# Kernel tuning notes

Measured on AMD Instinct MI355X. Metric: run time of the kernel, lower is better.

The kernel has to match this reference:

```python
import jax, jax.numpy as jnp
import numpy as np

_N_JOINTS = 24
_N_VERTS = 6890
_PARENT = np.array([-1, 0, 0, 0, 1, 2, 3, 4, 5, 6, 7, 8, 9, 9, 9, 12, 13, 14, 16, 17, 18, 19, 20, 21], dtype=np.int64)


def _batch_rodrigues(rvecs):
    # rvecs: [N,3] axis-angle -> [N,3,3] rotation matrices
    angle = jnp.clip(jnp.linalg.norm(rvecs, axis=-1, keepdims=True), 1e-8, None)
    axis = rvecs / angle
    a = angle[..., 0]
    c = jnp.cos(a)
    s = jnp.sin(a)
    t = 1.0 - c
    x, y, z = axis[:, 0], axis[:, 1], axis[:, 2]
    R = jnp.stack([
        t * x * x + c, t * x * y - s * z, t * x * z + s * y,
        t * x * y + s * z, t * y * y + c, t * y * z - s * x,
        t * x * z - s * y, t * y * z + s * x, t * z * z + c,
    ], axis=-1).reshape(-1, 3, 3)
    return R


def _make_T(R, trans):
    # R: [B,J,3,3], trans: [B,J,3] -> [B,J,4,4] homogeneous transforms
    B, J = R.shape[:2]
    top = jnp.concatenate([R, trans[..., None]], axis=-1)  # [B,J,3,4]
    bottom = jnp.broadcast_to(jnp.array([0.0, 0.0, 0.0, 1.0], dtype=R.dtype), (B, J, 1, 4))
    return jnp.concatenate([top, bottom], axis=2)


def setup_inputs() -> dict:
    key = jax.random.key(0)
    ks = jax.random.split(key, 7)
    B = 1024
    theta = jax.random.normal(ks[0], (B, 72), dtype=jnp.float32) * 0.3
    beta = jax.random.normal(ks[1], (B, 10), dtype=jnp.float32)
    shapedirs = jax.random.normal(ks[2], (_N_VERTS * 3, 10), dtype=jnp.float32) * 0.01
    posedirs = jax.random.normal(ks[3], (_N_VERTS * 3, 207), dtype=jnp.float32) * 0.01
    Jreg = jax.random.uniform(ks[4], (_N_JOINTS, _N_VERTS), dtype=jnp.float32)
    Jreg = Jreg / jnp.sum(Jreg, axis=1, keepdims=True)
    v_template = jax.random.normal(ks[5], (_N_VERTS, 3), dtype=jnp.float32)
    weights = jax.random.uniform(ks[6], (_N_VERTS, _N_JOINTS), dtype=jnp.float32)
    weights = weights / jnp.sum(weights, axis=1, keepdims=True)
    return {"theta": theta, "beta": beta, "shapedirs": shapedirs, "posedirs": posedirs,
            "J_regressor": Jreg, "v_template": v_template, "weights": weights}


def reference(theta, beta, shapedirs, posedirs, J_regressor, v_template, weights):
    B = beta.shape[0]
    V = v_template.shape[0]
    # shape blendshapes
    v_shaped = v_template[None] + (beta @ shapedirs.T).reshape(B, V, 3)
    # pose rotations
    R = _batch_rodrigues(theta.reshape(-1, 3)).reshape(B, _N_JOINTS, 3, 3)
    pose_feature = (R[:, 1:] - jnp.eye(3, dtype=R.dtype)).reshape(B, -1)  # [B,207]
    v_posed = v_shaped + (pose_feature @ posedirs.T).reshape(B, V, 3)
    # joint locations
    J = jnp.einsum('jv,bvk->bjk', J_regressor, v_posed)  # [B,24,3]
    # local bone transforms (root keeps absolute translation)
    Jp = J[:, np.maximum(_PARENT, 0)]                      # [B,24,3]
    rel = J - jnp.einsum('bjkl,bjl->bjk', R, Jp)
    is_root = (jnp.arange(_N_JOINTS) == 0)[None, :, None]
    trans = jnp.where(is_root, J, rel)
    T = _make_T(R, trans)                                  # [B,24,4,4]
    # kinematic chain accumulation (fixed 24-joint tree)
    Gs = [T[:, 0]]
    for i in range(1, _N_JOINTS):
        Gs.append(jnp.matmul(Gs[int(_PARENT[i])], T[:, i]))
    G = jnp.stack(Gs, axis=1)                              # [B,24,4,4]
    # remove rest-pose joint locations
    G_rot = G[:, :, :3, :3]
    G_tr = G[:, :, :3, 3] - jnp.einsum('bjkl,bjl->bjk', G_rot, J)
    G_corr = _make_T(G_rot, G_tr)                          # [B,24,4,4]
    # linear blend skinning
    T_skin = jnp.einsum('vj,bjkl->bvkl', weights, G_corr)  # [B,V,4,4]
    v_h = jnp.concatenate([v_posed, jnp.ones((B, V, 1), dtype=v_posed.dtype)], axis=-1)
    v_out = jnp.einsum('bvkl,bvl->bvk', T_skin, v_h)[:, :, :3]
    return v_out, J
```

## Files before the change

kernel.cpp:

```cpp
#include <hip/hip_runtime.h>
#include <hip/hip_bf16.h>

#define NJ 24
#define NV 6890
#define NVP 6912
#define NR (NV*3)
#define NPF 207
#define KB 217
#define KP 256
#define NT 162
#define NT2 108
#define NSPLIT 512
#define VPB 14
#define FTILE 32768
#define FT2   49152
#define ELDW 264

typedef short s16x8 __attribute__((ext_vector_type(8)));
typedef short s16x4 __attribute__((ext_vector_type(4)));
typedef float f32x4 __attribute__((ext_vector_type(4)));
typedef float f4u   __attribute__((ext_vector_type(4), aligned(4)));

__device__ constexpr int PAR[24] = {-1,0,0,0,1,2,3,4,5,6,7,8,9,9,9,12,13,14,16,17,18,19,20,21};

__device__ __forceinline__ short f2bf(float f) {
    __hip_bfloat16 h = __float2bfloat16(f);
    return *reinterpret_cast<short*>(&h);
}
__device__ __forceinline__ float bf2fs(unsigned short u) {
    unsigned int x = ((unsigned int)u) << 16;
    return __uint_as_float(x);
}

__device__ __forceinline__ size_t frag_addr(int row128, int k) {
    int ks = k >> 5, q = (k >> 3) & 3, e = k & 7;
    int mf = row128 >> 4, r16 = row128 & 15;
    return ((size_t)(ks*8 + mf) * 64 + q*16 + r16) * 8 + e;
}

__global__ __launch_bounds__(256) void k_rodrigues(const float* __restrict__ theta,
        const float* __restrict__ beta, float* __restrict__ Rws,
        float* __restrict__ pfA, short* __restrict__ Afrag, int B) {
    int idx = blockIdx.x * blockDim.x + threadIdx.x;
    if (idx >= B * NJ) return;
    int b = idx / NJ, j = idx % NJ;
    float x = theta[b*72 + j*3 + 0];
    float y = theta[b*72 + j*3 + 1];
    float z = theta[b*72 + j*3 + 2];
    float n = sqrtf(x*x + y*y + z*z);
    float a = fmaxf(n, 1e-8f);
    float inv = 1.0f / a;
    float ix = x*inv, iy = y*inv, iz = z*inv;
    float c = cosf(a), s = sinf(a), t = 1.0f - c;
    float r[9];
    r[0] = t*ix*ix + c;     r[1] = t*ix*iy - s*iz;  r[2] = t*ix*iz + s*iy;
    r[3] = t*ix*iy + s*iz;  r[4] = t*iy*iy + c;     r[5] = t*iy*iz - s*ix;
    r[6] = t*ix*iz - s*iy;  r[7] = t*iy*iz + s*ix;  r[8] = t*iz*iz + c;
    float* Rp = Rws + (size_t)idx * 9;
    #pragma unroll
    for (int k = 0; k < 9; ++k) Rp[k] = r[k];

    int rb = b & 127;
    short* At = Afrag + (size_t)(b >> 7) * FTILE;
    float* pa = pfA + (size_t)b * 224;
    if (j >= 1) {
        #pragma unroll
        for (int kk = 0; kk < 9; ++kk) {
            int k = (j-1)*9 + kk;
            float f = r[kk] - ((kk == 0 || kk == 4 || kk == 8) ? 1.0f : 0.0f);
            At[frag_addr(rb, k)] = f2bf(f);
            pa[k] = f;
        }
    } else {
        #pragma unroll
        for (int kk = 0; kk < 10; ++kk) {
            int k = NPF + kk;
            float f = beta[b*10 + kk];
            At[frag_addr(rb, k)] = f2bf(f);
            pa[k] = f;
        }
        for (int k = KB; k < KP; ++k)
            At[frag_addr(rb, k)] = 0;
    }
}

__global__ __launch_bounds__(256) void k_convB192(const float* __restrict__ pd,
        const float* __restrict__ sd, short* __restrict__ Bf) {
    int nt = blockIdx.y;
    int id = blockIdx.x * 256 + threadIdx.x;
    int lane_ = id & 63;
    int fi = id >> 6;
    int nf = fi % 12, ks = fi / 12;
    int q = lane_ >> 4, r16 = lane_ & 15;
    int rg = nt*192 + nf*16 + r16;
    int k0 = ks*32 + q*8;
    s16x8 v;
    if (rg < NR) {
        if (k0 + 7 < NPF) {
            const float* p = pd + (size_t)rg * NPF + k0;
            #pragma unroll
            for (int k = 0; k < 8; ++k) v[k] = f2bf(p[k]);
        } else {
            #pragma unroll
            for (int k = 0; k < 8; ++k) {
                int col = k0 + k;
                float f = 0.0f;
                if (col < NPF)     f = pd[(size_t)rg * NPF + col];
                else if (col < KB) f = sd[(size_t)rg * 10 + (col - NPF)];
                v[k] = f2bf(f);
            }
        }
    } else {
        #pragma unroll
        for (int k = 0; k < 8; ++k) v[k] = 0;
    }
    *(s16x8*)&Bf[((size_t)nt * FT2) + (size_t)id * 8] = v;
}

__global__ __launch_bounds__(256) void k_convB128(const float* __restrict__ pd,
        const float* __restrict__ sd, short* __restrict__ Bf) {
    int cid = blockIdx.x * 256 + threadIdx.x;
    int lane_ = cid & 63;
    int nf = (cid >> 6) & 7;
    int ks = (cid >> 9) & 7;
    int nt = cid >> 12;
    int q = lane_ >> 4, r16 = lane_ & 15;
    int rg = nt*128 + nf*16 + r16;
    int k0 = ks*32 + q*8;
    s16x8 v;
    if (rg < NR) {
        if (k0 + 7 < NPF) {
            const float* p = pd + (size_t)rg * NPF + k0;
            #pragma unroll
            for (int k = 0; k < 8; ++k) v[k] = f2bf(p[k]);
        } else {
            #pragma unroll
            for (int k = 0; k < 8; ++k) {
                int col = k0 + k;
                float f = 0.0f;
                if (col < NPF)     f = pd[(size_t)rg * NPF + col];
                else if (col < KB) f = sd[(size_t)rg * 10 + (col - NPF)];
                v[k] = f2bf(f);
            }
        }
    } else {
        #pragma unroll
        for (int k = 0; k < 8; ++k) v[k] = 0;
    }
    *(s16x8*)&Bf[(size_t)cid * 8] = v;
}

__global__ __launch_bounds__(256) void k_jdirs(const float* __restrict__ pd,
        const float* __restrict__ sd, const float* __restrict__ vt,
        const float* __restrict__ Jreg, float* __restrict__ part) {
    __shared__ float wjs[24][VPB];
    int bi = blockIdx.x;
    int v0 = bi * VPB;
    int nv = NV - v0; if (nv > VPB) nv = VPB; if (nv < 0) nv = 0;
    for (int i = threadIdx.x; i < 24*VPB; i += 256) {
        int j = i / VPB, vv = i - j*VPB;
        wjs[j][vv] = (vv < nv) ? Jreg[(size_t)j * NV + v0 + vv] : 0.0f;
    }
    __syncthreads();
    int k = threadIdx.x;
    float acc[72];
    #pragma unroll
    for (int i = 0; i < 72; ++i) acc[i] = 0.0f;
    for (int vv = 0; vv < VPB; ++vv) {
        int v = v0 + vv;
        if (v >= NV) break;
        #pragma unroll
        for (int c = 0; c < 3; ++c) {
            int row = v*3 + c;
            float val = 0.0f;
            if (k < NPF)      val = pd[(size_t)row * NPF + k];
            else if (k < KB)  val = sd[(size_t)row * 10 + (k - NPF)];
            else if (k == KB) val = vt[row];
            #pragma unroll
            for (int j = 0; j < 24; ++j) acc[j*3 + c] += wjs[j][vv] * val;
        }
    }
    if (k < 224) {
        float* p = part + (size_t)bi * (72*224);
        #pragma unroll
        for (int i = 0; i < 72; ++i) p[i*224 + k] = acc[i];
    }
}

__global__ __launch_bounds__(256) void k_jreduce1(const float* __restrict__ part,
        float* __restrict__ part2) {
    int i = blockIdx.x;
    int s = blockIdx.y;
    int k = threadIdx.x;
    if (k >= 224) return;
    float acc = 0.0f;
    #pragma unroll 4
    for (int bi = s*64; bi < s*64 + 64; ++bi)
        acc += part[(size_t)bi * (72*224) + i*224 + k];
    part2[((size_t)s * 72 + i) * 224 + k] = acc;
}

__global__ __launch_bounds__(256) void k_jreduce2(const float* __restrict__ part2,
        float* __restrict__ JDt) {
    int e = blockIdx.x * 256 + threadIdx.x;
    if (e >= 72*224) return;
    int i = e / 224, k = e - i*224;
    float s = 0.0f;
    #pragma unroll
    for (int ss = 0; ss < 8; ++ss)
        s += part2[((size_t)ss * 72 + i) * 224 + k];
    if (k < 218) JDt[k*72 + i] = s;
}

__global__ __launch_bounds__(128) void k_J(const float* __restrict__ pfA,
        const float* __restrict__ JDt, float* __restrict__ Jout, int B) {
    int b = blockIdx.x, t = threadIdx.x;
    if (t >= 72) return;
    const float* pa = pfA + (size_t)b * 224;
    float acc = JDt[217*72 + t];
    #pragma unroll 7
    for (int k = 0; k < KB; ++k) acc += pa[k] * JDt[k*72 + t];
    Jout[(size_t)b * 72 + t] = acc;
}

__global__ __launch_bounds__(32) void k_chain(const float* __restrict__ Rg,
        const float* __restrict__ Jg, float* __restrict__ Gc, int B) {
    __shared__ float Gs[32 * 289];
    int b = blockIdx.x * 32 + threadIdx.x;
    if (b >= B) return;
    float* G = &Gs[threadIdx.x * 289];
    float Jl[72];
    const float* Jb = Jg + (size_t)b * 72;
    #pragma unroll
    for (int i = 0; i < 72; ++i) Jl[i] = Jb[i];
    const float* Rb = Rg + (size_t)b * 216;
    G[0]=Rb[0]; G[1]=Rb[1]; G[2]=Rb[2];  G[3]=Jl[0];
    G[4]=Rb[3]; G[5]=Rb[4]; G[6]=Rb[5];  G[7]=Jl[1];
    G[8]=Rb[6]; G[9]=Rb[7]; G[10]=Rb[8]; G[11]=Jl[2];
    #pragma unroll
    for (int i = 1; i < NJ; ++i) {
        const int p = PAR[i];
        const float* Ri = Rb + i*9;
        float r00=Ri[0],r01=Ri[1],r02=Ri[2];
        float r10=Ri[3],r11=Ri[4],r12=Ri[5];
        float r20=Ri[6],r21=Ri[7],r22=Ri[8];
        float px=Jl[p*3+0], py=Jl[p*3+1], pz=Jl[p*3+2];
        float tx = Jl[i*3+0] - (r00*px + r01*py + r02*pz);
        float ty = Jl[i*3+1] - (r10*px + r11*py + r12*pz);
        float tz = Jl[i*3+2] - (r20*px + r21*py + r22*pz);
        const float* gp = &G[p*12];
        float* gi = &G[i*12];
        #pragma unroll
        for (int rr = 0; rr < 3; ++rr) {
            float a0=gp[rr*4+0], a1=gp[rr*4+1], a2=gp[rr*4+2], a3=gp[rr*4+3];
            gi[rr*4+0] = a0*r00 + a1*r10 + a2*r20;
            gi[rr*4+1] = a0*r01 + a1*r11 + a2*r21;
            gi[rr*4+2] = a0*r02 + a1*r12 + a2*r22;
            gi[rr*4+3] = a0*tx + a1*ty + a2*tz + a3;
        }
    }
    float* out = Gc + (size_t)b * 288;
    #pragma unroll
    for (int i = 0; i < NJ; ++i) {
        const float* gi = &G[i*12];
        float jx=Jl[i*3+0], jy=Jl[i*3+1], jz=Jl[i*3+2];
        #pragma unroll
        for (int rr = 0; rr < 3; ++rr) {
            out[i*12+rr*4+0] = gi[rr*4+0];
            out[i*12+rr*4+1] = gi[rr*4+1];
            out[i*12+rr*4+2] = gi[rr*4+2];
            out[i*12+rr*4+3] = gi[rr*4+3] - (gi[rr*4+0]*jx + gi[rr*4+1]*jy + gi[rr*4+2]*jz);
        }
    }
}

__global__ __launch_bounds__(256) void k_gmf(const float* __restrict__ Gc,
        short* __restrict__ Gmf, int B) {
    int idx = blockIdx.x * 256 + threadIdx.x;
    if (idx >= B * 64) return;
    int lane_ = idx & 63, b = idx >> 6;
    int q = lane_ >> 4, c = lane_ & 15;
    s16x8 v;
    if (c < 12 && q < 3) {
        #pragma unroll
        for (int e = 0; e < 8; ++e)
            v[e] = f2bf(Gc[(size_t)b * 288 + (q*8 + e)*12 + c]);
    } else {
        #pragma unroll
        for (int e = 0; e < 8; ++e) v[e] = 0;
    }
    *(s16x8*)&Gmf[(size_t)idx * 8] = v;
}

__global__ __launch_bounds__(256, 2) void k_gemm(const short* __restrict__ Af,
        const short* __restrict__ Bf, const float* __restrict__ vt,
        float* __restrict__ vout, int B) {
    __shared__ float eld[64 * 128];
    const int t = threadIdx.x;
    const int wgid = blockIdx.x;
    const int bt = wgid & 7, nt = wgid >> 3;
    const int wave = t >> 6, lane = t & 63;
    const int wn = (wave & 1) * 64;
    const int q = lane >> 4, r16 = lane & 15;
    const int mfb = (wave >> 1) * 4, nfb = (wave & 1) * 4;

    const s16x8* Ab = (const s16x8*)(Af + (size_t)bt * FTILE);
    const s16x8* Bb = (const s16x8*)(Bf + (size_t)nt * FTILE);

    f32x4 acc[4][4];
    #pragma unroll
    for (int m = 0; m < 4; ++m)
        #pragma unroll
        for (int n = 0; n < 4; ++n)
            #pragma unroll
            for (int i = 0; i < 4; ++i) acc[m][n][i] = 0.0f;

    #pragma unroll
    for (int ks = 0; ks < 8; ++ks) {
        s16x8 a[4], b[4];
        #pragma unroll
        for (int m = 0; m < 4; ++m) a[m] = Ab[(ks*8 + mfb + m)*64 + lane];
        #pragma unroll
        for (int n = 0; n < 4; ++n) b[n] = Bb[(ks*8 + nfb + n)*64 + lane];
        #pragma unroll
        for (int m = 0; m < 4; ++m)
            #pragma unroll
            for (int n = 0; n < 4; ++n)
                acc[m][n] = __builtin_amdgcn_mfma_f32_16x16x32_bf16(a[m], b[n], acc[m][n], 0, 0, 0);
    }

    #pragma unroll
    for (int half = 0; half < 2; ++half) {
        if ((wave >> 1) == half) {
            #pragma unroll
            for (int m = 0; m < 4; ++m)
                #pragma unroll
                for (int n = 0; n < 4; ++n)
                    #pragma unroll
                    for (int i = 0; i < 4; ++i) {
                        int row_l = m*16 + q*4 + i;
                        int col = wn + n*16 + r16;
                        eld[row_l * 128 + (col ^ ((row_l & 7) << 2))] = acc[m][n][i];
                    }
        }
        __syncthreads();
        {
            const int c32 = t & 31;
            const int col = c32 * 4;
            const int rsub = (t >> 5) & 1;
            #pragma unroll
            for (int it = 0; it < 8; ++it) {
                int row_l = it * 8 + wave * 2 + rsub;
                int bg = bt * 128 + half * 64 + row_l;
                int rg = nt * 128 + col;
                f32x4 v = *(const f32x4*)&eld[row_l * 128 + (col ^ ((row_l & 7) << 2))];
                if (bg < B) {
                    float* dst = vout + (size_t)bg * NR + rg;
                    if (rg + 3 < NR) {
                        float4 tv = *(const float4*)(vt + rg);
                        v[0] += tv.x; v[1] += tv.y; v[2] += tv.z; v[3] += tv.w;
                        *(f4u*)dst = v;
                    } else {
                        #pragma unroll
                        for (int e = 0; e < 4; ++e)
                            if (rg + e < NR) dst[e] = v[e] + vt[rg + e];
                    }
                }
            }
        }
        __syncthreads();
    }
}

__global__ __launch_bounds__(256, 2) void k_gemm_skin(const short* __restrict__ Af,
        const short* __restrict__ Bf, const float* __restrict__ vt,
        const short* __restrict__ Gmf, const float* __restrict__ W,
        float* __restrict__ vout, int B) {
    __shared__ short elds[128 * ELDW];
    const int t = threadIdx.x;
    const int wgid = blockIdx.x;
    const int bt = wgid & 7, nt = wgid >> 3;
    const int wave = t >> 6, lane = t & 63;
    const int wn = (wave & 1) * 96;
    const int q = lane >> 4, r16 = lane & 15;
    const int mfb = (wave >> 1) * 4, nfb = (wave & 1) * 6;
    const int rowbase = (wave >> 1) * 64;

    const s16x8* Ab = (const s16x8*)(Af + (size_t)bt * FTILE);
    const s16x8* Bb = (const s16x8*)(Bf + (size_t)nt * FT2);

    f32x4 acc[4][6];
    #pragma unroll
    for (int m = 0; m < 4; ++m)
        #pragma unroll
        for (int n = 0; n < 6; ++n)
            #pragma unroll
            for (int i = 0; i < 4; ++i) acc[m][n][i] = 0.0f;

    #pragma unroll
    for (int ks = 0; ks < 8; ++ks) {
        s16x8 a[4], b[6];
        #pragma unroll
        for (int m = 0; m < 4; ++m) a[m] = Ab[(ks*8 + mfb + m)*64 + lane];
        #pragma unroll
        for (int n = 0; n < 6; ++n) b[n] = Bb[(ks*12 + nfb + n)*64 + lane];
        #pragma unroll
        for (int m = 0; m < 4; ++m)
            #pragma unroll
            for (int n = 0; n < 6; ++n)
                acc[m][n] = __builtin_amdgcn_mfma_f32_16x16x32_bf16(a[m], b[n], acc[m][n], 0, 0, 0);
    }

    float vtv[6];
    int sofs[6];
    #pragma unroll
    for (int n = 0; n < 6; ++n) {
        int col = wn + n*16 + r16;
        int rg = nt*192 + col;
        vtv[n] = (rg < NR) ? vt[rg] : 0.0f;
        int vert = col / 3;
        sofs[n] = vert*4 + (col - vert*3);
    }

    s16x8 wf[4];
    int vert[4];
    bool vok[4];
    const int c16 = lane & 15;
    #pragma unroll
    for (int m = 0; m < 4; ++m) {
        vert[m] = nt*64 + m*16 + c16;
        vok[m] = (q < 3) && (vert[m] < NV);
        if (vok[m]) {
            const float* wp = W + (size_t)vert[m] * NJ + q*8;
            float4 f0 = *(const float4*)(wp);
            float4 f1 = *(const float4*)(wp + 4);
            wf[m][0]=f2bf(f0.x); wf[m][1]=f2bf(f0.y); wf[m][2]=f2bf(f0.z); wf[m][3]=f2bf(f0.w);
            wf[m][4]=f2bf(f1.x); wf[m][5]=f2bf(f1.y); wf[m][6]=f2bf(f1.z); wf[m][7]=f2bf(f1.w);
        } else {
            #pragma unroll
            for (int e = 0; e < 8; ++e) wf[m][e] = 0;
        }
    }

    #pragma unroll
    for (int m = 0; m < 4; ++m)
        #pragma unroll
        for (int i = 0; i < 4; ++i) {
            int row_l = rowbase + m*16 + q*4 + i;
            #pragma unroll
            for (int n = 0; n < 6; ++n)
                elds[row_l * ELDW + sofs[n]] = f2bf(acc[m][n][i] + vtv[n]);
        }
    __syncthreads();

    {
        s16x8 afA, afB;
        int bl0 = wave * 32;
        int bgbase = bt * 128;
        afA = *(const s16x8*)&Gmf[((size_t)(bgbase + bl0) * 64 + lane) * 8];
        #pragma unroll 8
        for (int bb = 0; bb < 32; ++bb) {
            if (bb + 1 < 32) {
                const s16x8* nx = (const s16x8*)&Gmf[((size_t)(bgbase + bl0 + bb + 1) * 64 + lane) * 8];
                if (bb & 1) afA = *nx; else afB = *nx;
            }
            s16x8 af = (bb & 1) ? afB : afA;
            int bl = bl0 + bb;
            int bg = bgbase + bl;
            #pragma unroll
            for (int m = 0; m < 4; ++m) {
                s16x4 vd = *(const s16x4*)&elds[bl * ELDW + (m*16 + c16) * 4];
                f32x4 zz = {0.0f, 0.0f, 0.0f, 0.0f};
                f32x4 Tq = __builtin_amdgcn_mfma_f32_16x16x32_bf16(af, wf[m], zz, 0, 0, 0);
                if (vok[m]) {
                    float x = bf2fs((unsigned short)vd[0]);
                    float y = bf2fs((unsigned short)vd[1]);
                    float z = bf2fs((unsigned short)vd[2]);
                    float o = Tq[0]*x + Tq[1]*y + Tq[2]*z + Tq[3];
                    vout[(size_t)bg * NR + (size_t)vert[m] * 3 + q] = o;
                }
            }
        }
    }
}

__global__ __launch_bounds__(256) void k_skin(float* __restrict__ vio,
        const float* __restrict__ W, const float* __restrict__ Gc, int B) {
    __shared__ short Gm[16 * 40];
    const int t = threadIdx.x;
    const int wave = t >> 6, lane = t & 63;
    const int q = lane >> 4, c = lane & 15;
    const int vb = blockIdx.x * 256 + wave * 64;
    const int b0 = blockIdx.y * 16;

    if (t < 320) ((int*)Gm)[t] = 0;

    s16x8 wf[4];
    #pragma unroll
    for (int m = 0; m < 4; ++m) {
        int vert = vb + m*16 + c;
        if (q < 3 && vert < NV) {
            const float* wp = W + (size_t)vert * NJ + q*8;
            float4 f0 = *(const float4*)(wp);
            float4 f1 = *(const float4*)(wp + 4);
            wf[m][0]=f2bf(f0.x); wf[m][1]=f2bf(f0.y); wf[m][2]=f2bf(f0.z); wf[m][3]=f2bf(f0.w);
            wf[m][4]=f2bf(f1.x); wf[m][5]=f2bf(f1.y); wf[m][6]=f2bf(f1.z); wf[m][7]=f2bf(f1.w);
        } else {
            #pragma unroll
            for (int e = 0; e < 8; ++e) wf[m][e] = 0;
        }
    }
    __syncthreads();

    for (int bb = 0; bb < 16; ++bb) {
        int b = b0 + bb;
        if (b >= B) break;
        {
            int i0 = t;
            int j0 = i0 / 12, c0 = i0 - j0*12;
            if (i0 < 288) Gm[c0*40 + j0] = f2bf(Gc[(size_t)b*288 + i0]);
            int i1 = t + 256;
            if (i1 < 288) {
                int j1 = i1 / 12, c1 = i1 - j1*12;
                Gm[c1*40 + j1] = f2bf(Gc[(size_t)b*288 + i1]);
            }
        }
        __syncthreads();

        s16x8 af = *(const s16x8*)&Gm[c*40 + q*8];
        #pragma unroll
        for (int m = 0; m < 4; ++m) {
            f32x4 zz = {0.0f, 0.0f, 0.0f, 0.0f};
            f32x4 acc = __builtin_amdgcn_mfma_f32_16x16x32_bf16(af, wf[m], zz, 0, 0, 0);
            int vert = vb + m*16 + c;
            bool ok = (q < 3) && (vert < NV);
            if (ok) {
                float* vp = vio + (size_t)b * NR + (size_t)vert * 3;
                float x = vp[0], y = vp[1], z = vp[2];
                float o = acc[0]*x + acc[1]*y + acc[2]*z + acc[3];
                vp[q] = o;
            }
        }
        __syncthreads();
    }
}

extern "C" void kernel_launch(void* const* d_in, const int* in_sizes, int n_in,
                              void* d_out, int out_size, void* d_ws, size_t ws_size,
                              hipStream_t stream) {
    const float* theta = (const float*)d_in[0];
    const float* beta  = (const float*)d_in[1];
    const float* sd    = (const float*)d_in[2];
    const float* pd    = (const float*)d_in[3];
    const float* Jreg  = (const float*)d_in[4];
    const float* vt    = (const float*)d_in[5];
    const float* W     = (const float*)d_in[6];
    float* out = (float*)d_out;

    const int B = in_sizes[0] / 72;

    float* vregion = out;
    float* Jout    = out + (size_t)B * NR;

    float* Rws   = (float*)d_ws;
    float* Gcws  = Rws + (size_t)B * 216;
    float* pfA   = Gcws + (size_t)B * 288;
    short* Afrag = (short*)(pfA + (size_t)B * 224);
    short* Bfrag = Afrag + (size_t)(B/128) * FTILE;
    short* Gmf   = Bfrag + (size_t)NT2 * FT2;

    size_t need_fuse = (size_t)B * 2912 + (size_t)(B/128) * FTILE * 2
                     + (size_t)NT2 * FT2 * 2 + (size_t)B * 512 * 2;
    const bool use_fuse = (ws_size >= need_fuse) && ((B & 127) == 0);

    float* part  = vregion;
    float* part2 = vregion + (size_t)NSPLIT * 72 * 224;
    float* JDt   = part2 + (size_t)8 * 72 * 224;

    k_rodrigues<<<(B*NJ + 255)/256, 256, 0, stream>>>(theta, beta, Rws, pfA, Afrag, B);
    if (use_fuse) {
        dim3 grid(24, NT2);
        k_convB192<<<grid, 256, 0, stream>>>(pd, sd, Bfrag);
    } else {
        k_convB128<<<(NT*8*8*64)/256, 256, 0, stream>>>(pd, sd, Bfrag);
    }
    k_jdirs<<<NSPLIT, 256, 0, stream>>>(pd, sd, vt, Jreg, part);
    {
        dim3 grid(72, 8);
        k_jreduce1<<<grid, 256, 0, stream>>>(part, part2);
    }
    k_jreduce2<<<(72*224 + 255)/256, 256, 0, stream>>>(part2, JDt);
    k_J<<<B, 128, 0, stream>>>(pfA, JDt, Jout, B);
    k_chain<<<(B + 31)/32, 32, 0, stream>>>(Rws, Jout, Gcws, B);

    if (use_fuse) {
        k_gmf<<<(B*64 + 255)/256, 256, 0, stream>>>(Gcws, Gmf, B);
        k_gemm_skin<<<NT2 * (B/128), 256, 0, stream>>>(Afrag, Bfrag, vt, Gmf, W, vregion, B);
    } else {
        k_gemm<<<NT * (B/128), 256, 0, stream>>>(Afrag, Bfrag, vt, vregion, B);
        dim3 grid((NV + 255)/256, (B + 15)/16);
        k_skin<<<grid, 256, 0, stream>>>(vregion, W, Gcws, B);
    }
}
```

Measured before the change: 125.6 us.

## Merge prep kernels into one launch and fold Gmf packing into chain kernel

Merges the independent rodrigues, B-fragment conversion and joint-direction partial kernels into a single k_prep launch that picks its role from the block index. This removes two launches and lets the three independent jobs run at the same time. The separate k_gmf kernel is removed: k_chain now applies the rest-pose correction in shared memory and writes the bf16 fragment layout directly. The cost is that k_chain now does serial, per-thread scattered 2-byte stores, and k_prep runs a heavier jdirs-style body (72 accumulators) in the same grid as lighter blocks.

New measurement: 114.4 us. 1.1x faster.

```diff
diff --git a/kernel.cpp b/kernel.cpp
--- a/kernel.cpp
+++ b/kernel.cpp
@@ -38,10 +38,9 @@
     return ((size_t)(ks*8 + mf) * 64 + q*16 + r16) * 8 + e;
 }
 
-__global__ __launch_bounds__(256) void k_rodrigues(const float* __restrict__ theta,
+__device__ __forceinline__ void rodrigues_body(int idx, const float* __restrict__ theta,
         const float* __restrict__ beta, float* __restrict__ Rws,
         float* __restrict__ pfA, short* __restrict__ Afrag, int B) {
-    int idx = blockIdx.x * blockDim.x + threadIdx.x;
     if (idx >= B * NJ) return;
     int b = idx / NJ, j = idx % NJ;
     float x = theta[b*72 + j*3 + 0];
@@ -84,10 +83,9 @@
     }
 }
 
-__global__ __launch_bounds__(256) void k_convB192(const float* __restrict__ pd,
-        const float* __restrict__ sd, short* __restrict__ Bf) {
-    int nt = blockIdx.y;
-    int id = blockIdx.x * 256 + threadIdx.x;
+__device__ __forceinline__ void convB192_body(int nt, int id,
+        const float* __restrict__ pd, const float* __restrict__ sd,
+        short* __restrict__ Bf) {
     int lane_ = id & 63;
     int fi = id >> 6;
     int nf = fi % 12, ks = fi / 12;
@@ -115,6 +113,64 @@
         for (int k = 0; k < 8; ++k) v[k] = 0;
     }
     *(s16x8*)&Bf[((size_t)nt * FT2) + (size_t)id * 8] = v;
+}
+
+__global__ __launch_bounds__(256) void k_prep(const float* __restrict__ theta,
+        const float* __restrict__ beta, const float* __restrict__ pd,
+        const float* __restrict__ sd, const float* __restrict__ vt,
+        const float* __restrict__ Jreg,
+        float* __restrict__ Rws, float* __restrict__ pfA, short* __restrict__ Afrag,
+        short* __restrict__ Bf, float* __restrict__ part, int B) {
+    __shared__ float wjs[24][VPB];
+    const int bid = blockIdx.x;
+    const int t = threadIdx.x;
+    if (bid < NSPLIT) {
+        int bi = bid;
+        int v0 = bi * VPB;
+        int nv = NV - v0; if (nv > VPB) nv = VPB; if (nv < 0) nv = 0;
+        for (int i = t; i < 24*VPB; i += 256) {
+            int j = i / VPB, vv = i - j*VPB;
+            wjs[j][vv] = (vv < nv) ? Jreg[(size_t)j * NV + v0 + vv] : 0.0f;
+        }
+        __syncthreads();
+        int k = t;
+        float acc[72];
+        #pragma unroll
+        for (int i = 0; i < 72; ++i) acc[i] = 0.0f;
+        for (int vv = 0; vv < VPB; ++vv) {
+            int v = v0 + vv;
+            if (v >= NV) break;
+            #pragma unroll
+            for (int c = 0; c < 3; ++c) {
+                int row = v*3 + c;
+                float val = 0.0f;
+                if (k < NPF)      val = pd[(size_t)row * NPF + k];
+                else if (k < KB)  val = sd[(size_t)row * 10 + (k - NPF)];
+                else if (k == KB) val = vt[row];
+                #pragma unroll
+                for (int j = 0; j < 24; ++j) acc[j*3 + c] += wjs[j][vv] * val;
+            }
+        }
+        if (k < 224) {
+            float* p = part + (size_t)bi * (72*224);
+            #pragma unroll
+            for (int i = 0; i < 72; ++i) p[i*224 + k] = acc[i];
+        }
+    } else if (bid < NSPLIT + 24*NT2) {
+        int cb = bid - NSPLIT;
+        int nt = cb / 24;
+        int id = (cb % 24) * 256 + t;
+        convB192_body(nt, id, pd, sd, Bf);
+    } else {
+        int idx = (bid - NSPLIT - 24*NT2) * 256 + t;
+        rodrigues_body(idx, theta, beta, Rws, pfA, Afrag, B);
+    }
+}
+
+__global__ __launch_bounds__(256) void k_rodrigues(const float* __restrict__ theta,
+        const float* __restrict__ beta, float* __restrict__ Rws,
+        float* __restrict__ pfA, short* __restrict__ Afrag, int B) {
+    rodrigues_body(blockIdx.x * blockDim.x + threadIdx.x, theta, beta, Rws, pfA, Afrag, B);
 }
 
 __global__ __launch_bounds__(256) void k_convB128(const float* __restrict__ pd,
@@ -224,7 +280,8 @@
 }
 
 __global__ __launch_bounds__(32) void k_chain(const float* __restrict__ Rg,
-        const float* __restrict__ Jg, float* __restrict__ Gc, int B) {
+        const float* __restrict__ Jg, float* __restrict__ Gc,
+        short* __restrict__ Gmf, int doGmf, int B) {
     __shared__ float Gs[32 * 289];
     int b = blockIdx.x * 32 + threadIdx.x;
     if (b >= B) return;
@@ -259,37 +316,36 @@
             gi[rr*4+3] = a0*tx + a1*ty + a2*tz + a3;
         }
     }
+    #pragma unroll
+    for (int i = 0; i < NJ; ++i) {
+        float* gi = &G[i*12];
+        float jx=Jl[i*3+0], jy=Jl[i*3+1], jz=Jl[i*3+2];
+        #pragma unroll
+        for (int rr = 0; rr < 3; ++rr)
+            gi[rr*4+3] = gi[rr*4+3] - (gi[rr*4+0]*jx + gi[rr*4+1]*jy + gi[rr*4+2]*jz);
+    }
     float* out = Gc + (size_t)b * 288;
     #pragma unroll
-    for (int i = 0; i < NJ; ++i) {
-        const float* gi = &G[i*12];
-        float jx=Jl[i*3+0], jy=Jl[i*3+1], jz=Jl[i*3+2];
-        #pragma unroll
-        for (int rr = 0; rr < 3; ++rr) {
-            out[i*12+rr*4+0] = gi[rr*4+0];
-            out[i*12+rr*4+1] = gi[rr*4+1];
-            out[i*12+rr*4+2] = gi[rr*4+2];
-            out[i*12+rr*4+3] = gi[rr*4+3] - (gi[rr*4+0]*jx + gi[rr*4+1]*jy + gi[rr*4+2]*jz);
-        }
-    }
-}
-
-__global__ __launch_bounds__(256) void k_gmf(const float* __restrict__ Gc,
-        short* __restrict__ Gmf, int B) {
-    int idx = blockIdx.x * 256 + threadIdx.x;
-    if (idx >= B * 64) return;
-    int lane_ = idx & 63, b = idx >> 6;
-    int q = lane_ >> 4, c = lane_ & 15;
-    s16x8 v;
-    if (c < 12 && q < 3) {
-        #pragma unroll
-        for (int e = 0; e < 8; ++e)
-            v[e] = f2bf(Gc[(size_t)b * 288 + (q*8 + e)*12 + c]);
-    } else {
-        #pragma unroll
-        for (int e = 0; e < 8; ++e) v[e] = 0;
-    }
-    *(s16x8*)&Gmf[(size_t)idx * 8] = v;
+    for (int i = 0; i < 288; ++i) out[i] = G[i];
+    if (doGmf) {
+        short* gm = Gmf + (size_t)b * 512;
+        #pragma unroll
+        for (int q = 0; q < 3; ++q)
+            for (int c = 0; c < 12; ++c) {
+                #pragma unroll
+                for (int e = 0; e < 8; ++e)
+                    gm[(q*16 + c)*8 + e] = f2bf(G[(q*8 + e)*12 + c]);
+            }
+        #pragma unroll
+        for (int q = 0; q < 3; ++q)
+            for (int c = 12; c < 16; ++c)
+                #pragma unroll
+                for (int e = 0; e < 8; ++e) gm[(q*16 + c)*8 + e] = 0;
+        #pragma unroll
+        for (int c = 0; c < 16; ++c)
+            #pragma unroll
+            for (int e = 0; e < 8; ++e) gm[(48 + c)*8 + e] = 0;
+    }
 }
 
 __global__ __launch_bounds__(256, 2) void k_gemm(const short* __restrict__ Af,
@@ -577,24 +633,25 @@
     float* part2 = vregion + (size_t)NSPLIT * 72 * 224;
     float* JDt   = part2 + (size_t)8 * 72 * 224;
 
-    k_rodrigues<<<(B*NJ + 255)/256, 256, 0, stream>>>(theta, beta, Rws, pfA, Afrag, B);
+    const int rodblocks = (B*NJ + 255)/256;
+
     if (use_fuse) {
-        dim3 grid(24, NT2);
-        k_convB192<<<grid, 256, 0, stream>>>(pd, sd, Bfrag);
+        k_prep<<<NSPLIT + 24*NT2 + rodblocks, 256, 0, stream>>>(
+            theta, beta, pd, sd, vt, Jreg, Rws, pfA, Afrag, Bfrag, part, B);
     } else {
+        k_rodrigues<<<rodblocks, 256, 0, stream>>>(theta, beta, Rws, pfA, Afrag, B);
         k_convB128<<<(NT*8*8*64)/256, 256, 0, stream>>>(pd, sd, Bfrag);
-    }
-    k_jdirs<<<NSPLIT, 256, 0, stream>>>(pd, sd, vt, Jreg, part);
+        k_jdirs<<<NSPLIT, 256, 0, stream>>>(pd, sd, vt, Jreg, part);
+    }
     {
         dim3 grid(72, 8);
         k_jreduce1<<<grid, 256, 0, stream>>>(part, part2);
     }
     k_jreduce2<<<(72*224 + 255)/256, 256, 0, stream>>>(part2, JDt);
     k_J<<<B, 128, 0, stream>>>(pfA, JDt, Jout, B);
-    k_chain<<<(B + 31)/32, 32, 0, stream>>>(Rws, Jout, Gcws, B);
+    k_chain<<<(B + 31)/32, 32, 0, stream>>>(Rws, Jout, Gcws, Gmf, use_fuse ? 1 : 0, B);
 
     if (use_fuse) {
-        k_gmf<<<(B*64 + 255)/256, 256, 0, stream>>>(Gcws, Gmf, B);
         k_gemm_skin<<<NT2 * (B/128), 256, 0, stream>>>(Afrag, Bfrag, vt, Gmf, W, vregion, B);
     } else {
         k_gemm<<<NT * (B/128), 256, 0, stream>>>(Afrag, Bfrag, vt, vregion, B);
```
